# Performance work log

Measured on AMD Instinct MI355X. Metric: run time of the kernel, lower is better.

The kernel has to match this reference:

```python
import jax, jax.numpy as jnp
import numpy as np

B, P, Q, H = 8, 2048, 512, 1024


def setup_inputs() -> dict:
    key = jax.random.key(0)
    k1, k2, k3, k4, k5 = jax.random.split(key, 5)
    passage = jax.random.normal(k1, (B, P, H), dtype=jnp.float32)
    question = jax.random.normal(k2, (B, Q, H), dtype=jnp.float32)
    q_mask = jax.random.randint(k3, (B, Q), 0, 2, dtype=jnp.int32)
    # map_linear params (torch Linear: y = x @ W.T + b)
    bound = 1.0 / np.sqrt(H)
    map_W = jax.random.uniform(k4, (H, H), jnp.float32, -bound, bound)
    map_b = jax.random.uniform(k5, (H,), jnp.float32, -bound, bound)
    return {"passage": passage, "question": question, "q_mask": q_mask,
            "map_W": map_W, "map_b": map_b}


def reference(passage, question, q_mask, map_W, map_b):
    # scores: [B, P, Q]
    scores = jnp.einsum("bph,bqh->bpq", passage, question)
    mask = q_mask.astype(scores.dtype)[:, None, :]  # [B, 1, Q], broadcasts over P
    # multiplicative masked softmax + renormalize (memory_efficient=False path)
    a = jax.nn.softmax(scores * mask, axis=-1) * mask
    alpha = a / (jnp.sum(a, axis=-1, keepdims=True) + 1e-13)
    # attend: [B, P, H]
    out = jnp.einsum("bpq,bqh->bph", alpha, question)
    # fused linear + ReLU
    return jax.nn.relu(jnp.einsum("bph,oh->bpo", out, map_W) + map_b)
```

## Files before the change

kernel.cpp:

```cpp
#include <hip/hip_runtime.h>
#include <hip/hip_bf16.h>

typedef __bf16 bf16;
typedef __bf16 bf16x8 __attribute__((ext_vector_type(8)));
typedef __bf16 bf16x4 __attribute__((ext_vector_type(4)));
typedef float  f32x4  __attribute__((ext_vector_type(4)));

#define B_ 8
#define P_ 2048
#define Q_ 512
#define H_ 1024

__device__ __forceinline__ void gload_lds16(const void* g, void* l) {
  __builtin_amdgcn_global_load_lds(
      (const __attribute__((address_space(1))) void*)g,
      (__attribute__((address_space(3))) void*)l, 16, 0, 0);
}

__global__ __launch_bounds__(256) void k_split(const float* __restrict__ x,
                                               bf16* __restrict__ hi,
                                               bf16* __restrict__ lo, int n4) {
  int i = blockIdx.x * blockDim.x + threadIdx.x;
  int stride = gridDim.x * blockDim.x;
  for (; i < n4; i += stride) {
    f32x4 v = ((const f32x4*)x)[i];
    bf16x4 h, l;
#pragma unroll
    for (int j = 0; j < 4; ++j) {
      bf16 hj = (bf16)v[j];
      h[j] = hj;
      l[j] = (bf16)(v[j] - (float)hj);
    }
    ((bf16x4*)hi)[i] = h;
    ((bf16x4*)lo)[i] = l;
  }
}

__global__ __launch_bounds__(256) void k_cvt(const float* __restrict__ x,
                                             bf16* __restrict__ y, int n4) {
  int i = blockIdx.x * blockDim.x + threadIdx.x;
  int stride = gridDim.x * blockDim.x;
  for (; i < n4; i += stride) {
    f32x4 v = ((const f32x4*)x)[i];
    bf16x4 h;
#pragma unroll
    for (int j = 0; j < 4; ++j) h[j] = (bf16)v[j];
    ((bf16x4*)y)[i] = h;
  }
}

__global__ __launch_bounds__(256) void k_transpose(const float* __restrict__ q,
                                                   bf16* __restrict__ qT) {
  __shared__ float t[64][65];
  int b = blockIdx.z;
  int h0 = blockIdx.x * 64, q0 = blockIdx.y * 64;
  int tid = threadIdx.x;
  int c4 = (tid & 15) * 4;
  int r16 = tid >> 4;
  const float* src = q + ((long)b * Q_ + q0) * H_ + h0;
#pragma unroll
  for (int i = 0; i < 4; ++i) {
    int r = r16 + i * 16;
    f32x4 v = *(const f32x4*)(src + (long)r * H_ + c4);
    t[c4 + 0][r] = v[0];
    t[c4 + 1][r] = v[1];
    t[c4 + 2][r] = v[2];
    t[c4 + 3][r] = v[3];
  }
  __syncthreads();
  bf16* dst = qT + ((long)b * H_ + h0) * Q_ + q0;
#pragma unroll
  for (int i = 0; i < 4; ++i) {
    int hr = r16 + i * 16;
    bf16x4 o;
#pragma unroll
    for (int j = 0; j < 4; ++j) o[j] = (bf16)t[hr][c4 + j];
    *(bf16x4*)(dst + (long)hr * Q_ + c4) = o;
  }
}

__global__ __launch_bounds__(512) void k_score_softmax(
    const float* __restrict__ passage, const bf16* __restrict__ q_hi,
    const bf16* __restrict__ q_lo, const int* __restrict__ qmask,
    bf16* __restrict__ alpha) {
  constexpr int NT = H_ / 32;
  constexpr int BUF = 36864;
  __shared__ __align__(16) bf16 smem[2 * BUF];

  int orig = blockIdx.x;
  int z = orig & 7;
  int row0 = (orig >> 3) * 64;

  int tid = threadIdx.x, wv = tid >> 6, lane = tid & 63;
  int fr = lane & 15;
  int kq = lane >> 4;
  int wr = (wv >> 2) * 32, wc = (wv & 3) * 128;
  int swz = (kq ^ ((fr >> 1) & 3)) * 8;

  const float* gA =
      passage + ((long)(z * P_ + row0 + (tid >> 3))) * H_ + (tid & 7) * 4;
  int aw = (tid >> 3) * 32 + ((((tid & 7) >> 1) ^ ((tid >> 4) & 3)) * 8) +
           (tid & 1) * 4;
  long broff = ((long)(z * Q_ + (tid >> 2))) * H_ +
               (((tid & 3) ^ ((tid >> 3) & 3)) * 8);
  const bf16* gBh = q_hi + broff;
  const bf16* gBl = q_lo + broff;
  int ldsBh = 4096 + wv * 512;
  int ldsBl = 20480 + wv * 512;

  auto stageB = [&](int t) {
    int bb = (t & 1) * BUF;
    const bf16* gh = gBh + t * 32;
    const bf16* gl = gBl + t * 32;
#pragma unroll
    for (int p = 0; p < 4; ++p)
      gload_lds16(gh + (long)p * 128 * H_, smem + bb + ldsBh + p * 4096);
#pragma unroll
    for (int p = 0; p < 4; ++p)
      gload_lds16(gl + (long)p * 128 * H_, smem + bb + ldsBl + p * 4096);
  };
  auto writeA = [&](int t, f32x4 av) {
    bf16x4 h, l;
#pragma unroll
    for (int j = 0; j < 4; ++j) {
      h[j] = (bf16)av[j];
      l[j] = (bf16)(av[j] - (float)h[j]);
    }
    int bb = (t & 1) * BUF;
    *(bf16x4*)(smem + bb + aw) = h;
    *(bf16x4*)(smem + bb + 2048 + aw) = l;
  };

  f32x4 acc[2][8] = {};
  auto compute = [&](int t) {
    const bf16* bb = smem + (t & 1) * BUF;
    bf16x8 ah[2], al[2], bh[8], bl[8];
#pragma unroll
    for (int m = 0; m < 2; ++m) {
      int ro = (wr + m * 16 + fr) * 32 + swz;
      ah[m] = *(const bf16x8*)(bb + ro);
      al[m] = *(const bf16x8*)(bb + 2048 + ro);
    }
#pragma unroll
    for (int n = 0; n < 8; ++n) {
      int ro = (wc + n * 16 + fr) * 32 + swz;
      bh[n] = *(const bf16x8*)(bb + 4096 + ro);
      bl[n] = *(const bf16x8*)(bb + 20480 + ro);
    }
#pragma unroll
    for (int m = 0; m < 2; ++m)
#pragma unroll
      for (int n = 0; n < 8; ++n) {
        acc[m][n] = __builtin_amdgcn_mfma_f32_16x16x32_bf16(ah[m], bh[n],
                                                            acc[m][n], 0, 0, 0);
        acc[m][n] = __builtin_amdgcn_mfma_f32_16x16x32_bf16(ah[m], bl[n],
                                                            acc[m][n], 0, 0, 0);
        acc[m][n] = __builtin_amdgcn_mfma_f32_16x16x32_bf16(al[m], bh[n],
                                                            acc[m][n], 0, 0, 0);
      }
  };

  {
    f32x4 a0 = *(const f32x4*)gA;
    stageB(0);
    writeA(0, a0);
    asm volatile("s_waitcnt vmcnt(0) lgkmcnt(0)" ::: "memory");
    __builtin_amdgcn_s_barrier();
    __builtin_amdgcn_sched_barrier(0);
  }
  for (int t = 0; t < NT; ++t) {
    f32x4 an;
    if (t < NT - 1) {
      an = *(const f32x4*)(gA + (t + 1) * 32);
      stageB(t + 1);
    }
    compute(t);
    if (t < NT - 1) {
      writeA(t + 1, an);
      asm volatile("s_waitcnt vmcnt(0) lgkmcnt(0)" ::: "memory");
      __builtin_amdgcn_s_barrier();
      __builtin_amdgcn_sched_barrier(0);
    }
  }

  float* red = (float*)smem;
  float* red2 = red + 256;
  const int* qm = qmask + z * Q_;
  float mk[8];
#pragma unroll
  for (int n = 0; n < 8; ++n) mk[n] = (float)qm[wc + n * 16 + fr];

  int rb = wr + (lane >> 4) * 4;
  float rmax[2][4];
#pragma unroll
  for (int m = 0; m < 2; ++m)
#pragma unroll
    for (int j = 0; j < 4; ++j) {
      float v = acc[m][0][j] * mk[0];
#pragma unroll
      for (int n = 1; n < 8; ++n) v = fmaxf(v, acc[m][n][j] * mk[n]);
      v = fmaxf(v, __shfl_xor(v, 1, 64));
      v = fmaxf(v, __shfl_xor(v, 2, 64));
      v = fmaxf(v, __shfl_xor(v, 4, 64));
      v = fmaxf(v, __shfl_xor(v, 8, 64));
      rmax[m][j] = v;
      if (fr == 0) red[(rb + m * 16 + j) * 4 + (wv & 3)] = v;
    }
  __syncthreads();
#pragma unroll
  for (int m = 0; m < 2; ++m)
#pragma unroll
    for (int j = 0; j < 4; ++j) {
      int r = rb + m * 16 + j;
      float v = fmaxf(fmaxf(red[r * 4], red[r * 4 + 1]),
                      fmaxf(red[r * 4 + 2], red[r * 4 + 3]));
      rmax[m][j] = v;
    }
  float Zp[2][4], Sp[2][4];
#pragma unroll
  for (int m = 0; m < 2; ++m)
#pragma unroll
    for (int j = 0; j < 4; ++j) {
      float zs = 0.f, ss = 0.f;
#pragma unroll
      for (int n = 0; n < 8; ++n) {
        float e = expf(acc[m][n][j] * mk[n] - rmax[m][j]);
        acc[m][n][j] = e;
        zs += e;
        ss += e * mk[n];
      }
      zs += __shfl_xor(zs, 1, 64); ss += __shfl_xor(ss, 1, 64);
      zs += __shfl_xor(zs, 2, 64); ss += __shfl_xor(ss, 2, 64);
      zs += __shfl_xor(zs, 4, 64); ss += __shfl_xor(ss, 4, 64);
      zs += __shfl_xor(zs, 8, 64); ss += __shfl_xor(ss, 8, 64);
      Zp[m][j] = zs;
      Sp[m][j] = ss;
      if (fr == 0) {
        red2[((rb + m * 16 + j) * 4 + (wv & 3)) * 2] = zs;
        red2[((rb + m * 16 + j) * 4 + (wv & 3)) * 2 + 1] = ss;
      }
    }
  __syncthreads();
  bf16* ap = alpha + ((long)(z * P_ + row0)) * Q_;
#pragma unroll
  for (int m = 0; m < 2; ++m)
#pragma unroll
    for (int j = 0; j < 4; ++j) {
      int r = rb + m * 16 + j;
      float Z = 0.f, Sm = 0.f;
#pragma unroll
      for (int w = 0; w < 4; ++w) {
        Z += red2[(r * 4 + w) * 2];
        Sm += red2[(r * 4 + w) * 2 + 1];
      }
      float inv = 1.0f / (Sm + 1e-13f * Z);
#pragma unroll
      for (int n = 0; n < 8; ++n)
        ap[(long)r * Q_ + wc + n * 16 + fr] =
            (bf16)(acc[m][n][j] * mk[n] * inv);
    }
}

template <int EPI, int NT>
__global__ __launch_bounds__(512, 2) void k_gemm256(
    const bf16* __restrict__ A, const bf16* __restrict__ Bm,
    void* __restrict__ Cv, const float* __restrict__ bias, int N, int gx,
    int gy, long sA, long sB, long sC) {
  constexpr int K = NT * 32;
  __shared__ __align__(16) bf16 smem[65536];

  int nwg = gridDim.x;
  int orig = blockIdx.x;
  int wg = (orig & 7) * (nwg >> 3) + (orig >> 3);
  int bx = wg % gx;
  int tt = wg / gx;
  int by = tt % gy;
  int z = tt / gy;
  int row0 = by * 256, col0 = bx * 256;
  A += z * sA;
  Bm += z * sB;

  int tid = threadIdx.x, wv = tid >> 6, lane = tid & 63;

  bool isA = wv < 4;
  int u0 = (wv & 3) * 4;
  int srow = u0 * 16 + (lane >> 2);
  int sclog = ((lane & 3) ^ ((lane >> 3) & 3)) * 8;
  const bf16* sbaseG = isA ? A + (long)(row0 + srow) * K + sclog
                           : Bm + (long)(col0 + srow) * K + sclog;
  int sbaseL = (isA ? 0 : 8192) + u0 * 512;

  auto stage = [&](int tile) {
    const bf16* g = sbaseG + tile * 32;
    bf16* l = smem + (tile & 3) * 16384 + sbaseL;
#pragma unroll
    for (int j = 0; j < 4; ++j) gload_lds16(g + (long)j * 16 * K, l + j * 512);
  };

  int wr = (wv >> 2) * 128, wc = (wv & 3) * 64;
  int fr = lane & 15, kq = lane >> 4;
  int swz = (kq ^ ((fr >> 1) & 3)) * 8 + fr * 32;

  f32x4 acc[8][4] = {};
  auto compute = [&](int t) {
    const bf16* bufA = smem + (t & 3) * 16384;
    const bf16* bufB = bufA + 8192;
    bf16x8 af[8], bfr[4];
#pragma unroll
    for (int m = 0; m < 8; ++m)
      af[m] = *(const bf16x8*)(bufA + (wr + m * 16) * 32 + swz);
#pragma unroll
    for (int n = 0; n < 4; ++n)
      bfr[n] = *(const bf16x8*)(bufB + (wc + n * 16) * 32 + swz);
#pragma unroll
    for (int m = 0; m < 8; ++m)
#pragma unroll
      for (int n = 0; n < 4; ++n)
        acc[m][n] = __builtin_amdgcn_mfma_f32_16x16x32_bf16(af[m], bfr[n],
                                                            acc[m][n], 0, 0, 0);
  };

  stage(0);
  stage(1);
  stage(2);
  asm volatile("s_waitcnt vmcnt(8)" ::: "memory");
  __builtin_amdgcn_s_barrier();
  __builtin_amdgcn_sched_barrier(0);
  for (int t = 0; t < NT - 3; ++t) {
    stage(t + 3);
    compute(t);
    asm volatile("s_waitcnt vmcnt(8)" ::: "memory");
    __builtin_amdgcn_s_barrier();
    __builtin_amdgcn_sched_barrier(0);
  }
  compute(NT - 3);
  asm volatile("s_waitcnt vmcnt(4)" ::: "memory");
  __builtin_amdgcn_s_barrier();
  __builtin_amdgcn_sched_barrier(0);
  compute(NT - 2);
  asm volatile("s_waitcnt vmcnt(0)" ::: "memory");
  __builtin_amdgcn_s_barrier();
  __builtin_amdgcn_sched_barrier(0);
  compute(NT - 1);

  int r0 = row0 + wr + (lane >> 4) * 4;
  int c0 = col0 + wc + fr;
  if constexpr (EPI == 1) {
    bf16* C = (bf16*)Cv + z * sC;
#pragma unroll
    for (int m = 0; m < 8; ++m)
#pragma unroll
      for (int n = 0; n < 4; ++n)
#pragma unroll
        for (int j = 0; j < 4; ++j)
          C[(long)(r0 + m * 16 + j) * N + c0 + n * 16] = (bf16)acc[m][n][j];
  } else {
    float* C = (float*)Cv;
#pragma unroll
    for (int n = 0; n < 4; ++n) {
      float bv = bias[c0 + n * 16];
#pragma unroll
      for (int m = 0; m < 8; ++m)
#pragma unroll
        for (int j = 0; j < 4; ++j) {
          float v = acc[m][n][j] + bv;
          C[(long)(r0 + m * 16 + j) * N + c0 + n * 16] = fmaxf(v, 0.f);
        }
    }
  }
}

extern "C" void kernel_launch(void* const* d_in, const int* in_sizes, int n_in,
                              void* d_out, int out_size, void* d_ws,
                              size_t ws_size, hipStream_t stream) {
  const float* passage = (const float*)d_in[0];
  const float* question = (const float*)d_in[1];
  const int* qmask = (const int*)d_in[2];
  const float* mapW = (const float*)d_in[3];
  const float* mapb = (const float*)d_in[4];

  char* ws = (char*)d_ws;
  size_t off = 0;
  auto alloc = [&](size_t bytes) {
    void* p = ws + off;
    off += (bytes + 255) & ~(size_t)255;
    return p;
  };
  bf16* q_hi = (bf16*)alloc((size_t)B_ * Q_ * H_ * 2);
  bf16* q_lo = (bf16*)alloc((size_t)B_ * Q_ * H_ * 2);
  bf16* qT = (bf16*)alloc((size_t)B_ * H_ * Q_ * 2);
  bf16* w_bf = (bf16*)alloc((size_t)H_ * H_ * 2);
  bf16* alpha = (bf16*)alloc((size_t)B_ * P_ * Q_ * 2);
  bf16* O = (bf16*)alloc((size_t)B_ * P_ * H_ * 2);

  k_split<<<1024, 256, 0, stream>>>(question, q_hi, q_lo, B_ * Q_ * H_ / 4);
  k_cvt<<<512, 256, 0, stream>>>(mapW, w_bf, H_ * H_ / 4);
  k_transpose<<<dim3(H_ / 64, Q_ / 64, B_), 256, 0, stream>>>(question, qT);

  k_score_softmax<<<256, 512, 0, stream>>>(passage, q_hi, q_lo, qmask, alpha);

  k_gemm256<1, Q_ / 32><<<256, 512, 0, stream>>>(
      alpha, qT, O, nullptr, H_, H_ / 256, P_ / 256, (long)P_ * Q_,
      (long)H_ * Q_, (long)P_ * H_);

  k_gemm256<2, H_ / 32><<<256, 512, 0, stream>>>(
      O, w_bf, d_out, mapb, H_, H_ / 256, (B_ * P_) / 256, 0, 0, 0);
}
```

Baseline: 144.4 us.

## Split score GEMM main loop into hi/lo B phases with finer-grained pipelining

Restructures the shared-memory layout of the score+softmax kernel so the A, B-hi and B-lo tiles each get separate double buffers. The K loop now runs in two half-phases. B-hi is loaded and used first while the B-lo copy for the next tile streams in, and passage rows are prefetched two steps ahead in registers. Partial vmcnt waits replace full drains, and s_setprio raises wave priority around the MFMA bursts. The aim is more overlap of global-to-LDS traffic with matrix math and fewer B register fragments live at once, at the cost of two barriers per iteration and delicate wait-count bookkeeping.

```diff
diff --git a/kernel.cpp b/kernel.cpp
--- a/kernel.cpp
+++ b/kernel.cpp
@@ -84,8 +84,7 @@
     const bf16* __restrict__ q_lo, const int* __restrict__ qmask,
     bf16* __restrict__ alpha) {
   constexpr int NT = H_ / 32;
-  constexpr int BUF = 36864;
-  __shared__ __align__(16) bf16 smem[2 * BUF];
+  __shared__ __align__(16) bf16 smem[73728];
 
   int orig = blockIdx.x;
   int z = orig & 7;
@@ -105,19 +104,20 @@
                (((tid & 3) ^ ((tid >> 3) & 3)) * 8);
   const bf16* gBh = q_hi + broff;
   const bf16* gBl = q_lo + broff;
-  int ldsBh = 4096 + wv * 512;
-  int ldsBl = 20480 + wv * 512;
-
-  auto stageB = [&](int t) {
-    int bb = (t & 1) * BUF;
-    const bf16* gh = gBh + t * 32;
-    const bf16* gl = gBl + t * 32;
+
+  auto stageBh = [&](int t) {
+    const bf16* g = gBh + t * 32;
+    bf16* l = smem + 8192 + (t & 1) * 16384 + wv * 512;
 #pragma unroll
     for (int p = 0; p < 4; ++p)
-      gload_lds16(gh + (long)p * 128 * H_, smem + bb + ldsBh + p * 4096);
+      gload_lds16(g + (long)p * 128 * H_, l + p * 4096);
+  };
+  auto stageBl = [&](int t) {
+    const bf16* g = gBl + t * 32;
+    bf16* l = smem + 40960 + (t & 1) * 16384 + wv * 512;
 #pragma unroll
     for (int p = 0; p < 4; ++p)
-      gload_lds16(gl + (long)p * 128 * H_, smem + bb + ldsBl + p * 4096);
+      gload_lds16(g + (long)p * 128 * H_, l + p * 4096);
   };
   auto writeA = [&](int t, f32x4 av) {
     bf16x4 h, l;
@@ -126,58 +126,82 @@
       h[j] = (bf16)av[j];
       l[j] = (bf16)(av[j] - (float)h[j]);
     }
-    int bb = (t & 1) * BUF;
+    int bb = (t & 1) * 4096;
     *(bf16x4*)(smem + bb + aw) = h;
     *(bf16x4*)(smem + bb + 2048 + aw) = l;
   };
 
   f32x4 acc[2][8] = {};
-  auto compute = [&](int t) {
-    const bf16* bb = smem + (t & 1) * BUF;
-    bf16x8 ah[2], al[2], bh[8], bl[8];
+  f32x4 areg[2];
+
+  areg[0] = *(const f32x4*)gA;
+  areg[1] = *(const f32x4*)(gA + 32);
+  stageBh(0);
+  stageBl(0);
+  writeA(0, areg[0]);
+  asm volatile("s_waitcnt vmcnt(4) lgkmcnt(0)" ::: "memory");
+  __builtin_amdgcn_s_barrier();
+  __builtin_amdgcn_sched_barrier(0);
+
+#pragma unroll
+  for (int t = 0; t < NT; ++t) {
+    const int par = t & 1;
+    const bf16* Ab = smem + par * 4096;
+    const bf16* Bhb = smem + 8192 + par * 16384;
+    const bf16* Blb = smem + 40960 + par * 16384;
+
+    bf16x8 ah[2], al[2], bq[8];
 #pragma unroll
     for (int m = 0; m < 2; ++m) {
       int ro = (wr + m * 16 + fr) * 32 + swz;
-      ah[m] = *(const bf16x8*)(bb + ro);
-      al[m] = *(const bf16x8*)(bb + 2048 + ro);
-    }
-#pragma unroll
-    for (int n = 0; n < 8; ++n) {
-      int ro = (wc + n * 16 + fr) * 32 + swz;
-      bh[n] = *(const bf16x8*)(bb + 4096 + ro);
-      bl[n] = *(const bf16x8*)(bb + 20480 + ro);
-    }
+      ah[m] = *(const bf16x8*)(Ab + ro);
+      al[m] = *(const bf16x8*)(Ab + 2048 + ro);
+    }
+#pragma unroll
+    for (int n = 0; n < 8; ++n)
+      bq[n] = *(const bf16x8*)(Bhb + (wc + n * 16 + fr) * 32 + swz);
+    if (t + 1 < NT) stageBh(t + 1);
+    if (t + 2 < NT) areg[par] = *(const f32x4*)(gA + (t + 2) * 32);
+    __builtin_amdgcn_s_setprio(1);
 #pragma unroll
     for (int m = 0; m < 2; ++m)
 #pragma unroll
       for (int n = 0; n < 8; ++n) {
-        acc[m][n] = __builtin_amdgcn_mfma_f32_16x16x32_bf16(ah[m], bh[n],
+        acc[m][n] = __builtin_amdgcn_mfma_f32_16x16x32_bf16(ah[m], bq[n],
                                                             acc[m][n], 0, 0, 0);
-        acc[m][n] = __builtin_amdgcn_mfma_f32_16x16x32_bf16(ah[m], bl[n],
-                                                            acc[m][n], 0, 0, 0);
-        acc[m][n] = __builtin_amdgcn_mfma_f32_16x16x32_bf16(al[m], bh[n],
+        acc[m][n] = __builtin_amdgcn_mfma_f32_16x16x32_bf16(al[m], bq[n],
                                                             acc[m][n], 0, 0, 0);
       }
-  };
-
-  {
-    f32x4 a0 = *(const f32x4*)gA;
-    stageB(0);
-    writeA(0, a0);
-    asm volatile("s_waitcnt vmcnt(0) lgkmcnt(0)" ::: "memory");
+    __builtin_amdgcn_s_setprio(0);
+    if (t < NT - 2)
+      asm volatile("s_waitcnt vmcnt(5) lgkmcnt(0)" ::: "memory");
+    else if (t == NT - 2)
+      asm volatile("s_waitcnt vmcnt(4) lgkmcnt(0)" ::: "memory");
+    else
+      asm volatile("s_waitcnt vmcnt(0) lgkmcnt(0)" ::: "memory");
     __builtin_amdgcn_s_barrier();
     __builtin_amdgcn_sched_barrier(0);
-  }
-  for (int t = 0; t < NT; ++t) {
-    f32x4 an;
-    if (t < NT - 1) {
-      an = *(const f32x4*)(gA + (t + 1) * 32);
-      stageB(t + 1);
-    }
-    compute(t);
-    if (t < NT - 1) {
-      writeA(t + 1, an);
-      asm volatile("s_waitcnt vmcnt(0) lgkmcnt(0)" ::: "memory");
+
+#pragma unroll
+    for (int n = 0; n < 8; ++n)
+      bq[n] = *(const bf16x8*)(Blb + (wc + n * 16 + fr) * 32 + swz);
+    if (t + 1 < NT) {
+      writeA(t + 1, areg[(t + 1) & 1]);
+      stageBl(t + 1);
+    }
+    __builtin_amdgcn_s_setprio(1);
+#pragma unroll
+    for (int m = 0; m < 2; ++m)
+#pragma unroll
+      for (int n = 0; n < 8; ++n)
+        acc[m][n] = __builtin_amdgcn_mfma_f32_16x16x32_bf16(ah[m], bq[n],
+                                                            acc[m][n], 0, 0, 0);
+    __builtin_amdgcn_s_setprio(0);
+    if (t + 1 < NT) {
+      if (t < NT - 2)
+        asm volatile("s_waitcnt vmcnt(5) lgkmcnt(0)" ::: "memory");
+      else
+        asm volatile("s_waitcnt vmcnt(4) lgkmcnt(0)" ::: "memory");
       __builtin_amdgcn_s_barrier();
       __builtin_amdgcn_sched_barrier(0);
     }
@@ -212,11 +236,9 @@
 #pragma unroll
     for (int j = 0; j < 4; ++j) {
       int r = rb + m * 16 + j;
-      float v = fmaxf(fmaxf(red[r * 4], red[r * 4 + 1]),
-                      fmaxf(red[r * 4 + 2], red[r * 4 + 3]));
-      rmax[m][j] = v;
-    }
-  float Zp[2][4], Sp[2][4];
+      rmax[m][j] = fmaxf(fmaxf(red[r * 4], red[r * 4 + 1]),
+                         fmaxf(red[r * 4 + 2], red[r * 4 + 3]));
+    }
 #pragma unroll
   for (int m = 0; m < 2; ++m)
 #pragma unroll
@@ -233,8 +255,6 @@
       zs += __shfl_xor(zs, 2, 64); ss += __shfl_xor(ss, 2, 64);
       zs += __shfl_xor(zs, 4, 64); ss += __shfl_xor(ss, 4, 64);
       zs += __shfl_xor(zs, 8, 64); ss += __shfl_xor(ss, 8, 64);
-      Zp[m][j] = zs;
-      Sp[m][j] = ss;
       if (fr == 0) {
         red2[((rb + m * 16 + j) * 4 + (wv & 3)) * 2] = zs;
         red2[((rb + m * 16 + j) * 4 + (wv & 3)) * 2 + 1] = ss;
```

New measurement: 136.3 us. 5.6% less time.

## Switch to single-pass fp16 MFMA and retile score-softmax kernel

Applied to the files above, without the earlier changes.

Replaces the bf16 hi/lo split (three MFMAs per tile) in the score kernel with a single fp16 MFMA pass, and converts all intermediates and GEMMs to fp16. The score kernel is retiled to 32 rows per block with 512 blocks and two blocks per CU, using a smaller LDS footprint, register prefetch of passage tiles and s_setprio around the MFMAs. The separate split kernel is removed and the fp16 question copy is produced inside the transpose kernel. This cuts MFMA work and memory traffic, but fp16 has only about 11 bits of mantissa and a limited range, so the raw scores (sums over 1024 products of normal values) lose accuracy compared with the split scheme.

```diff
diff --git a/kernel.cpp b/kernel.cpp
--- a/kernel.cpp
+++ b/kernel.cpp
@@ -1,10 +1,12 @@
 #include <hip/hip_runtime.h>
 #include <hip/hip_bf16.h>
 
-typedef __bf16 bf16;
-typedef __bf16 bf16x8 __attribute__((ext_vector_type(8)));
-typedef __bf16 bf16x4 __attribute__((ext_vector_type(4)));
-typedef float  f32x4  __attribute__((ext_vector_type(4)));
+typedef _Float16 f16;
+typedef _Float16 f16x8 __attribute__((ext_vector_type(8)));
+typedef _Float16 f16x4 __attribute__((ext_vector_type(4)));
+typedef _Float16 f16x2 __attribute__((ext_vector_type(2)));
+typedef float f32x4 __attribute__((ext_vector_type(4)));
+typedef float f32x2 __attribute__((ext_vector_type(2)));
 
 #define B_ 8
 #define P_ 2048
@@ -17,40 +19,22 @@
       (__attribute__((address_space(3))) void*)l, 16, 0, 0);
 }
 
-__global__ __launch_bounds__(256) void k_split(const float* __restrict__ x,
-                                               bf16* __restrict__ hi,
-                                               bf16* __restrict__ lo, int n4) {
+__global__ __launch_bounds__(256) void k_cvt16(const float* __restrict__ x,
+                                               f16* __restrict__ y, int n4) {
   int i = blockIdx.x * blockDim.x + threadIdx.x;
   int stride = gridDim.x * blockDim.x;
   for (; i < n4; i += stride) {
     f32x4 v = ((const f32x4*)x)[i];
-    bf16x4 h, l;
-#pragma unroll
-    for (int j = 0; j < 4; ++j) {
-      bf16 hj = (bf16)v[j];
-      h[j] = hj;
-      l[j] = (bf16)(v[j] - (float)hj);
-    }
-    ((bf16x4*)hi)[i] = h;
-    ((bf16x4*)lo)[i] = l;
-  }
-}
-
-__global__ __launch_bounds__(256) void k_cvt(const float* __restrict__ x,
-                                             bf16* __restrict__ y, int n4) {
-  int i = blockIdx.x * blockDim.x + threadIdx.x;
-  int stride = gridDim.x * blockDim.x;
-  for (; i < n4; i += stride) {
-    f32x4 v = ((const f32x4*)x)[i];
-    bf16x4 h;
-#pragma unroll
-    for (int j = 0; j < 4; ++j) h[j] = (bf16)v[j];
-    ((bf16x4*)y)[i] = h;
+    f16x4 h;
+#pragma unroll
+    for (int j = 0; j < 4; ++j) h[j] = (f16)v[j];
+    ((f16x4*)y)[i] = h;
   }
 }
 
 __global__ __launch_bounds__(256) void k_transpose(const float* __restrict__ q,
-                                                   bf16* __restrict__ qT) {
+                                                   f16* __restrict__ qT,
+                                                   f16* __restrict__ q16) {
   __shared__ float t[64][65];
   int b = blockIdx.z;
   int h0 = blockIdx.x * 64, q0 = blockIdx.y * 64;
@@ -58,139 +42,125 @@
   int c4 = (tid & 15) * 4;
   int r16 = tid >> 4;
   const float* src = q + ((long)b * Q_ + q0) * H_ + h0;
+  f16* d16 = q16 + ((long)b * Q_ + q0) * H_ + h0;
 #pragma unroll
   for (int i = 0; i < 4; ++i) {
     int r = r16 + i * 16;
     f32x4 v = *(const f32x4*)(src + (long)r * H_ + c4);
+    f16x4 s;
+#pragma unroll
+    for (int j = 0; j < 4; ++j) s[j] = (f16)v[j];
+    *(f16x4*)(d16 + (long)r * H_ + c4) = s;
     t[c4 + 0][r] = v[0];
     t[c4 + 1][r] = v[1];
     t[c4 + 2][r] = v[2];
     t[c4 + 3][r] = v[3];
   }
   __syncthreads();
-  bf16* dst = qT + ((long)b * H_ + h0) * Q_ + q0;
+  f16* dst = qT + ((long)b * H_ + h0) * Q_ + q0;
 #pragma unroll
   for (int i = 0; i < 4; ++i) {
     int hr = r16 + i * 16;
-    bf16x4 o;
-#pragma unroll
-    for (int j = 0; j < 4; ++j) o[j] = (bf16)t[hr][c4 + j];
-    *(bf16x4*)(dst + (long)hr * Q_ + c4) = o;
-  }
-}
-
-__global__ __launch_bounds__(512) void k_score_softmax(
-    const float* __restrict__ passage, const bf16* __restrict__ q_hi,
-    const bf16* __restrict__ q_lo, const int* __restrict__ qmask,
-    bf16* __restrict__ alpha) {
+    f16x4 o;
+#pragma unroll
+    for (int j = 0; j < 4; ++j) o[j] = (f16)t[hr][c4 + j];
+    *(f16x4*)(dst + (long)hr * Q_ + c4) = o;
+  }
+}
+
+__global__ __launch_bounds__(512, 2) void k_score_softmax(
+    const float* __restrict__ passage, const f16* __restrict__ q16,
+    const int* __restrict__ qmask, f16* __restrict__ alpha) {
   constexpr int NT = H_ / 32;
-  constexpr int BUF = 36864;
-  __shared__ __align__(16) bf16 smem[2 * BUF];
+  __shared__ __align__(16) f16 smem[2048 + 32768];
 
   int orig = blockIdx.x;
   int z = orig & 7;
-  int row0 = (orig >> 3) * 64;
+  int row0 = (orig >> 3) * 32;
 
   int tid = threadIdx.x, wv = tid >> 6, lane = tid & 63;
-  int fr = lane & 15;
-  int kq = lane >> 4;
-  int wr = (wv >> 2) * 32, wc = (wv & 3) * 128;
+  int fr = lane & 15, kq = lane >> 4;
+  int wc = wv * 64;
   int swz = (kq ^ ((fr >> 1) & 3)) * 8;
 
-  const float* gA =
-      passage + ((long)(z * P_ + row0 + (tid >> 3))) * H_ + (tid & 7) * 4;
-  int aw = (tid >> 3) * 32 + ((((tid & 7) >> 1) ^ ((tid >> 4) & 3)) * 8) +
-           (tid & 1) * 4;
-  long broff = ((long)(z * Q_ + (tid >> 2))) * H_ +
-               (((tid & 3) ^ ((tid >> 3) & 3)) * 8);
-  const bf16* gBh = q_hi + broff;
-  const bf16* gBl = q_lo + broff;
-  int ldsBh = 4096 + wv * 512;
-  int ldsBl = 20480 + wv * 512;
+  int arow = tid >> 4;
+  int acol2 = (tid & 15) * 2;
+  const float* gA = passage + ((long)(z * P_ + row0 + arow)) * H_ + acol2;
+  int aw = arow * 32 + ((acol2 >> 3) ^ ((arow >> 1) & 3)) * 8 + (acol2 & 7);
+
+  const f16* gB = q16 + ((long)(z * Q_ + (tid >> 2))) * H_ +
+                  (((tid & 3) ^ ((tid >> 3) & 3)) * 8);
 
   auto stageB = [&](int t) {
-    int bb = (t & 1) * BUF;
-    const bf16* gh = gBh + t * 32;
-    const bf16* gl = gBl + t * 32;
+    const f16* g = gB + t * 32;
+    f16* l = smem + 2048 + (t & 1) * 16384 + wv * 512;
 #pragma unroll
     for (int p = 0; p < 4; ++p)
-      gload_lds16(gh + (long)p * 128 * H_, smem + bb + ldsBh + p * 4096);
-#pragma unroll
-    for (int p = 0; p < 4; ++p)
-      gload_lds16(gl + (long)p * 128 * H_, smem + bb + ldsBl + p * 4096);
-  };
-  auto writeA = [&](int t, f32x4 av) {
-    bf16x4 h, l;
-#pragma unroll
-    for (int j = 0; j < 4; ++j) {
-      h[j] = (bf16)av[j];
-      l[j] = (bf16)(av[j] - (float)h[j]);
-    }
-    int bb = (t & 1) * BUF;
-    *(bf16x4*)(smem + bb + aw) = h;
-    *(bf16x4*)(smem + bb + 2048 + aw) = l;
-  };
-
-  f32x4 acc[2][8] = {};
-  auto compute = [&](int t) {
-    const bf16* bb = smem + (t & 1) * BUF;
-    bf16x8 ah[2], al[2], bh[8], bl[8];
-#pragma unroll
-    for (int m = 0; m < 2; ++m) {
-      int ro = (wr + m * 16 + fr) * 32 + swz;
-      ah[m] = *(const bf16x8*)(bb + ro);
-      al[m] = *(const bf16x8*)(bb + 2048 + ro);
-    }
-#pragma unroll
-    for (int n = 0; n < 8; ++n) {
-      int ro = (wc + n * 16 + fr) * 32 + swz;
-      bh[n] = *(const bf16x8*)(bb + 4096 + ro);
-      bl[n] = *(const bf16x8*)(bb + 20480 + ro);
-    }
+      gload_lds16(g + (long)p * 128 * H_, l + p * 4096);
+  };
+  auto writeA = [&](int t, f32x2 av) {
+    f16x2 h;
+    h[0] = (f16)av[0];
+    h[1] = (f16)av[1];
+    *(f16x2*)(smem + (t & 1) * 1024 + aw) = h;
+  };
+
+  f32x4 acc[2][4] = {};
+  f32x2 areg0, areg1;
+
+  areg0 = *(const f32x2*)gA;
+  stageB(0);
+  areg1 = *(const f32x2*)(gA + 32);
+  writeA(0, areg0);
+  asm volatile("s_waitcnt vmcnt(1) lgkmcnt(0)" ::: "memory");
+  __builtin_amdgcn_s_barrier();
+  __builtin_amdgcn_sched_barrier(0);
+
+#pragma unroll 2
+  for (int t = 0; t < NT; ++t) {
+    if (t + 1 < NT) stageB(t + 1);
+    f16x8 af[2], bf[4];
+    const f16* Ab = smem + (t & 1) * 1024;
+    const f16* Bb = smem + 2048 + (t & 1) * 16384;
 #pragma unroll
     for (int m = 0; m < 2; ++m)
-#pragma unroll
-      for (int n = 0; n < 8; ++n) {
-        acc[m][n] = __builtin_amdgcn_mfma_f32_16x16x32_bf16(ah[m], bh[n],
-                                                            acc[m][n], 0, 0, 0);
-        acc[m][n] = __builtin_amdgcn_mfma_f32_16x16x32_bf16(ah[m], bl[n],
-                                                            acc[m][n], 0, 0, 0);
-        acc[m][n] = __builtin_amdgcn_mfma_f32_16x16x32_bf16(al[m], bh[n],
-                                                            acc[m][n], 0, 0, 0);
-      }
-  };
-
-  {
-    f32x4 a0 = *(const f32x4*)gA;
-    stageB(0);
-    writeA(0, a0);
-    asm volatile("s_waitcnt vmcnt(0) lgkmcnt(0)" ::: "memory");
-    __builtin_amdgcn_s_barrier();
-    __builtin_amdgcn_sched_barrier(0);
-  }
-  for (int t = 0; t < NT; ++t) {
-    f32x4 an;
+      af[m] = *(const f16x8*)(Ab + (m * 16 + fr) * 32 + swz);
+#pragma unroll
+    for (int n = 0; n < 4; ++n)
+      bf[n] = *(const f16x8*)(Bb + (wc + n * 16 + fr) * 32 + swz);
+    if (t + 1 < NT)
+      writeA(t + 1, ((t + 1) & 1) ? areg1 : areg0);
+    if (t + 2 < NT) {
+      f32x2 a = *(const f32x2*)(gA + (t + 2) * 32);
+      if ((t + 2) & 1) areg1 = a; else areg0 = a;
+    }
+    __builtin_amdgcn_s_setprio(1);
+#pragma unroll
+    for (int m = 0; m < 2; ++m)
+#pragma unroll
+      for (int n = 0; n < 4; ++n)
+        acc[m][n] = __builtin_amdgcn_mfma_f32_16x16x32_f16(af[m], bf[n],
+                                                           acc[m][n], 0, 0, 0);
+    __builtin_amdgcn_s_setprio(0);
+    if (t < NT - 2)
+      asm volatile("s_waitcnt vmcnt(1) lgkmcnt(0)" ::: "memory");
+    else if (t == NT - 2)
+      asm volatile("s_waitcnt vmcnt(0) lgkmcnt(0)" ::: "memory");
     if (t < NT - 1) {
-      an = *(const f32x4*)(gA + (t + 1) * 32);
-      stageB(t + 1);
-    }
-    compute(t);
-    if (t < NT - 1) {
-      writeA(t + 1, an);
-      asm volatile("s_waitcnt vmcnt(0) lgkmcnt(0)" ::: "memory");
       __builtin_amdgcn_s_barrier();
       __builtin_amdgcn_sched_barrier(0);
     }
   }
 
+  __syncthreads();
   float* red = (float*)smem;
   float* red2 = red + 256;
   const int* qm = qmask + z * Q_;
-  float mk[8];
-#pragma unroll
-  for (int n = 0; n < 8; ++n) mk[n] = (float)qm[wc + n * 16 + fr];
-
-  int rb = wr + (lane >> 4) * 4;
+  float mk[4];
+#pragma unroll
+  for (int n = 0; n < 4; ++n) mk[n] = (float)qm[wc + n * 16 + fr];
+
+  int rb = (lane >> 4) * 4;
   float rmax[2][4];
 #pragma unroll
   for (int m = 0; m < 2; ++m)
@@ -198,13 +168,12 @@
     for (int j = 0; j < 4; ++j) {
       float v = acc[m][0][j] * mk[0];
 #pragma unroll
-      for (int n = 1; n < 8; ++n) v = fmaxf(v, acc[m][n][j] * mk[n]);
+      for (int n = 1; n < 4; ++n) v = fmaxf(v, acc[m][n][j] * mk[n]);
       v = fmaxf(v, __shfl_xor(v, 1, 64));
       v = fmaxf(v, __shfl_xor(v, 2, 64));
       v = fmaxf(v, __shfl_xor(v, 4, 64));
       v = fmaxf(v, __shfl_xor(v, 8, 64));
-      rmax[m][j] = v;
-      if (fr == 0) red[(rb + m * 16 + j) * 4 + (wv & 3)] = v;
+      if (fr == 0) red[(rb + m * 16 + j) * 8 + wv] = v;
     }
   __syncthreads();
 #pragma unroll
@@ -212,18 +181,18 @@
 #pragma unroll
     for (int j = 0; j < 4; ++j) {
       int r = rb + m * 16 + j;
-      float v = fmaxf(fmaxf(red[r * 4], red[r * 4 + 1]),
-                      fmaxf(red[r * 4 + 2], red[r * 4 + 3]));
+      float v = red[r * 8];
+#pragma unroll
+      for (int w = 1; w < 8; ++w) v = fmaxf(v, red[r * 8 + w]);
       rmax[m][j] = v;
     }
-  float Zp[2][4], Sp[2][4];
 #pragma unroll
   for (int m = 0; m < 2; ++m)
 #pragma unroll
     for (int j = 0; j < 4; ++j) {
       float zs = 0.f, ss = 0.f;
 #pragma unroll
-      for (int n = 0; n < 8; ++n) {
+      for (int n = 0; n < 4; ++n) {
         float e = expf(acc[m][n][j] * mk[n] - rmax[m][j]);
         acc[m][n][j] = e;
         zs += e;
@@ -233,15 +202,13 @@
       zs += __shfl_xor(zs, 2, 64); ss += __shfl_xor(ss, 2, 64);
       zs += __shfl_xor(zs, 4, 64); ss += __shfl_xor(ss, 4, 64);
       zs += __shfl_xor(zs, 8, 64); ss += __shfl_xor(ss, 8, 64);
-      Zp[m][j] = zs;
-      Sp[m][j] = ss;
       if (fr == 0) {
-        red2[((rb + m * 16 + j) * 4 + (wv & 3)) * 2] = zs;
-        red2[((rb + m * 16 + j) * 4 + (wv & 3)) * 2 + 1] = ss;
+        red2[((rb + m * 16 + j) * 8 + wv) * 2] = zs;
+        red2[((rb + m * 16 + j) * 8 + wv) * 2 + 1] = ss;
       }
     }
   __syncthreads();
-  bf16* ap = alpha + ((long)(z * P_ + row0)) * Q_;
+  f16* ap = alpha + ((long)(z * P_ + row0)) * Q_;
 #pragma unroll
   for (int m = 0; m < 2; ++m)
 #pragma unroll
@@ -249,25 +216,24 @@
       int r = rb + m * 16 + j;
       float Z = 0.f, Sm = 0.f;
 #pragma unroll
-      for (int w = 0; w < 4; ++w) {
-        Z += red2[(r * 4 + w) * 2];
-        Sm += red2[(r * 4 + w) * 2 + 1];
+      for (int w = 0; w < 8; ++w) {
+        Z += red2[(r * 8 + w) * 2];
+        Sm += red2[(r * 8 + w) * 2 + 1];
       }
       float inv = 1.0f / (Sm + 1e-13f * Z);
 #pragma unroll
-      for (int n = 0; n < 8; ++n)
-        ap[(long)r * Q_ + wc + n * 16 + fr] =
-            (bf16)(acc[m][n][j] * mk[n] * inv);
+      for (int n = 0; n < 4; ++n)
+        ap[(long)r * Q_ + wc + n * 16 + fr] = (f16)(acc[m][n][j] * mk[n] * inv);
     }
 }
 
 template <int EPI, int NT>
 __global__ __launch_bounds__(512, 2) void k_gemm256(
-    const bf16* __restrict__ A, const bf16* __restrict__ Bm,
+    const f16* __restrict__ A, const f16* __restrict__ Bm,
     void* __restrict__ Cv, const float* __restrict__ bias, int N, int gx,
     int gy, long sA, long sB, long sC) {
   constexpr int K = NT * 32;
-  __shared__ __align__(16) bf16 smem[65536];
+  __shared__ __align__(16) f16 smem[65536];
 
   int nwg = gridDim.x;
   int orig = blockIdx.x;
@@ -286,13 +252,13 @@
   int u0 = (wv & 3) * 4;
   int srow = u0 * 16 + (lane >> 2);
   int sclog = ((lane & 3) ^ ((lane >> 3) & 3)) * 8;
-  const bf16* sbaseG = isA ? A + (long)(row0 + srow) * K + sclog
-                           : Bm + (long)(col0 + srow) * K + sclog;
+  const f16* sbaseG = isA ? A + (long)(row0 + srow) * K + sclog
+                          : Bm + (long)(col0 + srow) * K + sclog;
   int sbaseL = (isA ? 0 : 8192) + u0 * 512;
 
   auto stage = [&](int tile) {
-    const bf16* g = sbaseG + tile * 32;
-    bf16* l = smem + (tile & 3) * 16384 + sbaseL;
+    const f16* g = sbaseG + (long)tile * 32;
+    f16* l = smem + (tile & 3) * 16384 + sbaseL;
 #pragma unroll
     for (int j = 0; j < 4; ++j) gload_lds16(g + (long)j * 16 * K, l + j * 512);
   };
@@ -303,21 +269,21 @@
 
   f32x4 acc[8][4] = {};
   auto compute = [&](int t) {
-    const bf16* bufA = smem + (t & 3) * 16384;
-    const bf16* bufB = bufA + 8192;
-    bf16x8 af[8], bfr[4];
+    const f16* bufA = smem + (t & 3) * 16384;
+    const f16* bufB = bufA + 8192;
+    f16x8 af[8], bfr[4];
 #pragma unroll
     for (int m = 0; m < 8; ++m)
-      af[m] = *(const bf16x8*)(bufA + (wr + m * 16) * 32 + swz);
+      af[m] = *(const f16x8*)(bufA + (wr + m * 16) * 32 + swz);
 #pragma unroll
     for (int n = 0; n < 4; ++n)
-      bfr[n] = *(const bf16x8*)(bufB + (wc + n * 16) * 32 + swz);
+      bfr[n] = *(const f16x8*)(bufB + (wc + n * 16) * 32 + swz);
 #pragma unroll
     for (int m = 0; m < 8; ++m)
 #pragma unroll
       for (int n = 0; n < 4; ++n)
-        acc[m][n] = __builtin_amdgcn_mfma_f32_16x16x32_bf16(af[m], bfr[n],
-                                                            acc[m][n], 0, 0, 0);
+        acc[m][n] = __builtin_amdgcn_mfma_f32_16x16x32_f16(af[m], bfr[n],
+                                                           acc[m][n], 0, 0, 0);
   };
 
   stage(0);
@@ -346,14 +312,14 @@
   int r0 = row0 + wr + (lane >> 4) * 4;
   int c0 = col0 + wc + fr;
   if constexpr (EPI == 1) {
-    bf16* C = (bf16*)Cv + z * sC;
+    f16* C = (f16*)Cv + z * sC;
 #pragma unroll
     for (int m = 0; m < 8; ++m)
 #pragma unroll
       for (int n = 0; n < 4; ++n)
 #pragma unroll
         for (int j = 0; j < 4; ++j)
-          C[(long)(r0 + m * 16 + j) * N + c0 + n * 16] = (bf16)acc[m][n][j];
+          C[(long)(r0 + m * 16 + j) * N + c0 + n * 16] = (f16)acc[m][n][j];
   } else {
     float* C = (float*)Cv;
 #pragma unroll
@@ -386,23 +352,22 @@
     off += (bytes + 255) & ~(size_t)255;
     return p;
   };
-  bf16* q_hi = (bf16*)alloc((size_t)B_ * Q_ * H_ * 2);
-  bf16* q_lo = (bf16*)alloc((size_t)B_ * Q_ * H_ * 2);
-  bf16* qT = (bf16*)alloc((size_t)B_ * H_ * Q_ * 2);
-  bf16* w_bf = (bf16*)alloc((size_t)H_ * H_ * 2);
-  bf16* alpha = (bf16*)alloc((size_t)B_ * P_ * Q_ * 2);
-  bf16* O = (bf16*)alloc((size_t)B_ * P_ * H_ * 2);
-
-  k_split<<<1024, 256, 0, stream>>>(question, q_hi, q_lo, B_ * Q_ * H_ / 4);
-  k_cvt<<<512, 256, 0, stream>>>(mapW, w_bf, H_ * H_ / 4);
-  k_transpose<<<dim3(H_ / 64, Q_ / 64, B_), 256, 0, stream>>>(question, qT);
-
-  k_score_softmax<<<256, 512, 0, stream>>>(passage, q_hi, q_lo, qmask, alpha);
+  f16* q16 = (f16*)alloc((size_t)B_ * Q_ * H_ * 2);
+  f16* qT = (f16*)alloc((size_t)B_ * H_ * Q_ * 2);
+  f16* w16 = (f16*)alloc((size_t)H_ * H_ * 2);
+  f16* alpha = (f16*)alloc((size_t)B_ * P_ * Q_ * 2);
+  f16* O = (f16*)alloc((size_t)B_ * P_ * H_ * 2);
+
+  k_cvt16<<<512, 256, 0, stream>>>(mapW, w16, H_ * H_ / 4);
+  k_transpose<<<dim3(H_ / 64, Q_ / 64, B_), 256, 0, stream>>>(question, qT,
+                                                              q16);
+
+  k_score_softmax<<<512, 512, 0, stream>>>(passage, q16, qmask, alpha);
 
   k_gemm256<1, Q_ / 32><<<256, 512, 0, stream>>>(
       alpha, qT, O, nullptr, H_, H_ / 256, P_ / 256, (long)P_ * Q_,
       (long)H_ * Q_, (long)P_ * H_);
 
   k_gemm256<2, H_ / 32><<<256, 512, 0, stream>>>(
-      O, w_bf, d_out, mapb, H_, H_ / 256, (B_ * P_) / 256, 0, 0, 0);
-}
+      O, w16, d_out, mapb, H_, H_ / 256, (B_ * P_) / 256, 0, 0, 0);
+}
```

Result: faster. 121.6 us (-15.8%).
